# Kernel tuning notes

Measured on AMD Instinct MI355X. Metric: run time of the kernel, lower is better.

The kernel has to match this reference:

```python
import jax, jax.numpy as jnp
import numpy as np

IN_FEATURES = 4096
UNITS = 4096
BATCH = 8192
DENSITY = 0.1
NNZ = int(DENSITY * IN_FEATURES * UNITS)  # 1677721


def _make_indices(rng):
    """Mimic full='output' index construction: each column gets
    NNZ//UNITS distinct random rows; a random 'remain' subset of columns
    gets one extra row. Indices are unique (no duplicates)."""
    k = NNZ // UNITS
    rem = NNZ % UNITS
    # random row permutation per column: argsort of uniform noise
    perm = np.argsort(rng.random((UNITS, IN_FEATURES)), axis=1)
    rows_base = perm[:, :k].reshape(-1)                      # [UNITS*k]
    cols_base = np.repeat(np.arange(UNITS), k)               # [UNITS*k]
    rem_cols = rng.choice(UNITS, rem, replace=False)
    rows_extra = perm[rem_cols, k]
    rows = np.concatenate([rows_base, rows_extra]).astype(np.int32)
    cols = np.concatenate([cols_base, rem_cols]).astype(np.int32)
    return rows, cols


def setup_inputs() -> dict:
    rng = np.random.default_rng(0)
    rows, cols = _make_indices(rng)
    key = jax.random.key(0)
    k1, k2 = jax.random.split(key)
    x = jax.random.normal(k1, (BATCH, IN_FEATURES), dtype=jnp.float32)
    # glorot-uniform-ish scale for the sparse values
    kernel = jax.random.normal(k2, (NNZ,), dtype=jnp.float32) * 0.02
    bias = jnp.zeros((UNITS,), dtype=jnp.float32)
    return {"x": x, "kernel": kernel, "bias": bias,
            "rows": jnp.asarray(rows), "cols": jnp.asarray(cols)}


def reference(x, kernel, bias, rows, cols):
    in_features = x.shape[-1]
    units = bias.shape[0]
    # Scatter sparse COO values into the dense [in, units] weight
    # (indices are unique, so .set is exact), then dense matmul ==
    # tf.sparse.sparse_dense_matmul with the same values/indices.
    W = jnp.zeros((in_features, units), dtype=x.dtype).at[rows, cols].set(kernel)
    out = x @ W + bias
    return jax.nn.relu(out)
```

## Files before the change

kernel.cpp:

```cpp
#include <hip/hip_runtime.h>
#include <hip/hip_bf16.h>

typedef __bf16 bf16;
typedef __attribute__((ext_vector_type(8))) __bf16 bf16x8;
typedef __attribute__((ext_vector_type(4))) __bf16 bf16x4;
typedef __attribute__((ext_vector_type(4))) float f32x4;

#define IN_F 4096
#define UNITS 4096
#define BATCH 8192
#define NNZ_CNT 1677721

#define BM 128
#define BN 128
#define BK 32
#define GK IN_F

#define GLOAD_LDS16(g, l)                                              \
  __builtin_amdgcn_global_load_lds(                                    \
      (const __attribute__((address_space(1))) void*)(g),              \
      (__attribute__((address_space(3))) void*)(l), 16, 0, 0)

__global__ __launch_bounds__(256) void scatter_w_kernel(
    const float* __restrict__ vals, const int* __restrict__ rows,
    const int* __restrict__ cols, bf16* __restrict__ Wt) {
  int i = blockIdx.x * 256 + threadIdx.x;
  if (i < NNZ_CNT) {
    Wt[(size_t)cols[i] * IN_F + rows[i]] = (bf16)vals[i];
  }
}

__global__ __launch_bounds__(256) void cvt_x_kernel(
    const float* __restrict__ x, bf16* __restrict__ xb) {
  size_t i = ((size_t)blockIdx.x * 256 + threadIdx.x) * 4;
  float4 v = *(const float4*)(x + i);
  bf16x4 b;
  b.x = (bf16)v.x;
  b.y = (bf16)v.y;
  b.z = (bf16)v.z;
  b.w = (bf16)v.w;
  *(bf16x4*)(xb + i) = b;
}

__global__ __launch_bounds__(256) void gemm_bias_relu_kernel(
    const bf16* __restrict__ A, const bf16* __restrict__ Bt,
    const float* __restrict__ bias, float* __restrict__ C) {
  __shared__ bf16 As[BM * BK];
  __shared__ bf16 Bs[BN * BK];

  const int tid = threadIdx.x;
  const int lane = tid & 63;
  const int wave = tid >> 6;
  const int wm = wave >> 1;
  const int wn = wave & 1;

  const long m0 = (long)blockIdx.y * BM;
  const long n0 = (long)blockIdx.x * BN;

  const int e0 = tid;
  const int e1 = tid + 256;
  const bf16* gA0 = A + (m0 + (e0 >> 2)) * (long)GK + (e0 & 3) * 8;
  const bf16* gA1 = A + (m0 + (e1 >> 2)) * (long)GK + (e1 & 3) * 8;
  const bf16* gB0 = Bt + (n0 + (e0 >> 2)) * (long)GK + (e0 & 3) * 8;
  const bf16* gB1 = Bt + (n0 + (e1 >> 2)) * (long)GK + (e1 & 3) * 8;

  const int frow = lane & 15;
  const int fk = (lane >> 4) * 8;
  const bf16* lA = As + (wm * 64 + frow) * BK + fk;
  const bf16* lB = Bs + (wn * 64 + frow) * BK + fk;

  f32x4 acc[4][4] = {};

  for (int kt = 0; kt < GK; kt += BK) {
    __syncthreads();
    GLOAD_LDS16(gA0 + kt, As + e0 * 8);
    GLOAD_LDS16(gA1 + kt, As + e1 * 8);
    GLOAD_LDS16(gB0 + kt, Bs + e0 * 8);
    GLOAD_LDS16(gB1 + kt, Bs + e1 * 8);
    __syncthreads();

    bf16x8 af[4], bfr[4];
#pragma unroll
    for (int i = 0; i < 4; ++i) af[i] = *(const bf16x8*)(lA + i * 16 * BK);
#pragma unroll
    for (int i = 0; i < 4; ++i) bfr[i] = *(const bf16x8*)(lB + i * 16 * BK);

#pragma unroll
    for (int im = 0; im < 4; ++im)
#pragma unroll
      for (int in = 0; in < 4; ++in)
        acc[im][in] = __builtin_amdgcn_mfma_f32_16x16x32_bf16(
            af[im], bfr[in], acc[im][in], 0, 0, 0);
  }

  const int crow = (lane >> 4) * 4;
  const int ccol = lane & 15;
#pragma unroll
  for (int in = 0; in < 4; ++in) {
    const long n = n0 + wn * 64 + in * 16 + ccol;
    const float bv = bias[n];
#pragma unroll
    for (int im = 0; im < 4; ++im) {
      const long mbase = m0 + wm * 64 + im * 16 + crow;
#pragma unroll
      for (int i = 0; i < 4; ++i) {
        float v = acc[im][in][i] + bv;
        C[(mbase + i) * UNITS + n] = v > 0.f ? v : 0.f;
      }
    }
  }
}

extern "C" void kernel_launch(void* const* d_in, const int* in_sizes, int n_in,
                              void* d_out, int out_size, void* d_ws,
                              size_t ws_size, hipStream_t stream) {
  const float* x = (const float*)d_in[0];
  const float* kern = (const float*)d_in[1];
  const float* bias = (const float*)d_in[2];
  const int* rows = (const int*)d_in[3];
  const int* cols = (const int*)d_in[4];
  float* out = (float*)d_out;

  bf16* Wt = (bf16*)d_ws;
  bf16* xb = (bf16*)((char*)d_ws + (size_t)UNITS * IN_F * sizeof(bf16));

  hipMemsetAsync(Wt, 0, (size_t)UNITS * IN_F * sizeof(bf16), stream);

  scatter_w_kernel<<<(NNZ_CNT + 255) / 256, 256, 0, stream>>>(kern, rows, cols,
                                                              Wt);

  cvt_x_kernel<<<(size_t)BATCH * IN_F / 4 / 256, 256, 0, stream>>>(x, xb);

  dim3 grid(UNITS / BN, BATCH / BM);
  gemm_bias_relu_kernel<<<grid, 256, 0, stream>>>(xb, Wt, bias, out);
}
```

Before: 575.3 us.

## Replace GEMM with 256x256-tile 8-wave double-buffered pipelined kernel

Swaps the simple 128x128 single-buffered GEMM for a 256x256-tile kernel using 8 waves, XOR-swizzled LDS, and double-buffered global-to-LDS staging. Loads are interleaved with MFMA quads and paced by explicit barriers, vmcnt waits and setprio. Blocks are remapped for L2 locality and the x-conversion kernel now handles 8 elements per thread. It uses 128KB of LDS per block, which limits occupancy, and its correctness depends on the hand-written wait and barrier sequence.

```diff
diff --git a/kernel.cpp b/kernel.cpp
--- a/kernel.cpp
+++ b/kernel.cpp
@@ -3,23 +3,24 @@
 
 typedef __bf16 bf16;
 typedef __attribute__((ext_vector_type(8))) __bf16 bf16x8;
-typedef __attribute__((ext_vector_type(4))) __bf16 bf16x4;
 typedef __attribute__((ext_vector_type(4))) float f32x4;
 
 #define IN_F 4096
 #define UNITS 4096
 #define BATCH 8192
 #define NNZ_CNT 1677721
-
-#define BM 128
-#define BN 128
-#define BK 32
-#define GK IN_F
+#define NT 64
+#define NITER 32
 
 #define GLOAD_LDS16(g, l)                                              \
   __builtin_amdgcn_global_load_lds(                                    \
       (const __attribute__((address_space(1))) void*)(g),              \
       (__attribute__((address_space(3))) void*)(l), 16, 0, 0)
+
+#define S_BARRIER() asm volatile("s_barrier" ::: "memory")
+#define VMCNT4() asm volatile("s_waitcnt vmcnt(4)" ::: "memory")
+#define PRIO1() __builtin_amdgcn_s_setprio(1)
+#define PRIO0() __builtin_amdgcn_s_setprio(0)
 
 __global__ __launch_bounds__(256) void scatter_w_kernel(
     const float* __restrict__ vals, const int* __restrict__ rows,
@@ -30,85 +31,160 @@
   }
 }
 
-__global__ __launch_bounds__(256) void cvt_x_kernel(
-    const float* __restrict__ x, bf16* __restrict__ xb) {
-  size_t i = ((size_t)blockIdx.x * 256 + threadIdx.x) * 4;
-  float4 v = *(const float4*)(x + i);
-  bf16x4 b;
-  b.x = (bf16)v.x;
-  b.y = (bf16)v.y;
-  b.z = (bf16)v.z;
-  b.w = (bf16)v.w;
-  *(bf16x4*)(xb + i) = b;
-}
-
-__global__ __launch_bounds__(256) void gemm_bias_relu_kernel(
+__global__ __launch_bounds__(256) void cvt_x_kernel(const float* __restrict__ x,
+                                                    bf16* __restrict__ xb) {
+  size_t i = ((size_t)blockIdx.x * 256 + threadIdx.x) * 8;
+  float4 v0 = *(const float4*)(x + i);
+  float4 v1 = *(const float4*)(x + i + 4);
+  bf16x8 o;
+  o[0] = (bf16)v0.x; o[1] = (bf16)v0.y; o[2] = (bf16)v0.z; o[3] = (bf16)v0.w;
+  o[4] = (bf16)v1.x; o[5] = (bf16)v1.y; o[6] = (bf16)v1.z; o[7] = (bf16)v1.w;
+  *(bf16x8*)(xb + i) = o;
+}
+
+__device__ __forceinline__ void stage2(const bf16* s0, bf16* l, int tid) {
+  GLOAD_LDS16(s0, l + tid * 8);
+  GLOAD_LDS16(s0 + 128 * (long)IN_F, l + 4096 + tid * 8);
+}
+
+template <int MH, int NH>
+__device__ __forceinline__ void mfma_quad(const bf16x8 (&a)[8],
+                                          const bf16x8 (&b)[2][4],
+                                          f32x4 (&acc)[8][4]) {
+#pragma unroll
+  for (int im = 0; im < 4; ++im)
+#pragma unroll
+    for (int in = 0; in < 2; ++in)
+#pragma unroll
+      for (int ks = 0; ks < 2; ++ks)
+        acc[MH * 4 + im][NH * 2 + in] =
+            __builtin_amdgcn_mfma_f32_16x16x32_bf16(
+                a[im * 2 + ks], b[NH][in * 2 + ks],
+                acc[MH * 4 + im][NH * 2 + in], 0, 0, 0);
+}
+
+__global__ __launch_bounds__(512, 2) void gemm8_kernel(
     const bf16* __restrict__ A, const bf16* __restrict__ Bt,
     const float* __restrict__ bias, float* __restrict__ C) {
-  __shared__ bf16 As[BM * BK];
-  __shared__ bf16 Bs[BN * BK];
+  __shared__ bf16 lds[65536];
 
   const int tid = threadIdx.x;
   const int lane = tid & 63;
   const int wave = tid >> 6;
-  const int wm = wave >> 1;
-  const int wn = wave & 1;
-
-  const long m0 = (long)blockIdx.y * BM;
-  const long n0 = (long)blockIdx.x * BN;
-
-  const int e0 = tid;
-  const int e1 = tid + 256;
-  const bf16* gA0 = A + (m0 + (e0 >> 2)) * (long)GK + (e0 & 3) * 8;
-  const bf16* gA1 = A + (m0 + (e1 >> 2)) * (long)GK + (e1 & 3) * 8;
-  const bf16* gB0 = Bt + (n0 + (e0 >> 2)) * (long)GK + (e0 & 3) * 8;
-  const bf16* gB1 = Bt + (n0 + (e1 >> 2)) * (long)GK + (e1 & 3) * 8;
-
-  const int frow = lane & 15;
-  const int fk = (lane >> 4) * 8;
-  const bf16* lA = As + (wm * 64 + frow) * BK + fk;
-  const bf16* lB = Bs + (wn * 64 + frow) * BK + fk;
-
-  f32x4 acc[4][4] = {};
-
-  for (int kt = 0; kt < GK; kt += BK) {
-    __syncthreads();
-    GLOAD_LDS16(gA0 + kt, As + e0 * 8);
-    GLOAD_LDS16(gA1 + kt, As + e1 * 8);
-    GLOAD_LDS16(gB0 + kt, Bs + e0 * 8);
-    GLOAD_LDS16(gB1 + kt, Bs + e1 * 8);
-    __syncthreads();
-
-    bf16x8 af[4], bfr[4];
-#pragma unroll
-    for (int i = 0; i < 4; ++i) af[i] = *(const bf16x8*)(lA + i * 16 * BK);
-#pragma unroll
-    for (int i = 0; i < 4; ++i) bfr[i] = *(const bf16x8*)(lB + i * 16 * BK);
-
-#pragma unroll
-    for (int im = 0; im < 4; ++im)
-#pragma unroll
-      for (int in = 0; in < 4; ++in)
-        acc[im][in] = __builtin_amdgcn_mfma_f32_16x16x32_bf16(
-            af[im], bfr[in], acc[im][in], 0, 0, 0);
-  }
-
-  const int crow = (lane >> 4) * 4;
-  const int ccol = lane & 15;
-#pragma unroll
-  for (int in = 0; in < 4; ++in) {
-    const long n = n0 + wn * 64 + in * 16 + ccol;
+  const int wm = wave >> 2;
+  const int wn = wave & 3;
+
+  const int sb = (blockIdx.x & 7) * 64 + (blockIdx.x >> 3);
+  const long m0 = (long)(sb & 31) * 256;
+  const long n0 = (long)(sb >> 5) * 256;
+
+  const int q = tid >> 3;
+  const int kx = ((tid & 7) << 3) ^ ((q & 7) << 3);
+  const bf16* gA = A + (m0 + q) * (long)IN_F + kx;
+  const bf16* gB = Bt + (n0 + (q >> 5) * 64 + (q & 31)) * (long)IN_F + kx;
+
+  const int kA0 = (((lane >> 4) << 3) ^ ((lane & 7) << 3));
+  const int baseA = (wm * 64 + (lane & 15)) * 64;
+  const int baseB = (wn * 32 + (lane & 15)) * 64;
+
+  bf16x8 a[8];
+  bf16x8 b[2][4];
+  f32x4 acc[8][4] = {};
+
+#define LDSA(buf, h) (lds + ((buf) * 4 + (h)) * 8192)
+#define LDSB(buf, h) (lds + ((buf) * 4 + 2 + (h)) * 8192)
+#define STAGE_A(buf, h, kt) \
+  stage2(gA + (h) * 64 * (long)IN_F + (kt) * 64, LDSA(buf, h), tid)
+#define STAGE_B(buf, h, kt) \
+  stage2(gB + (h) * 32 * (long)IN_F + (kt) * 64, LDSB(buf, h), tid)
+#define LOAD_A(buf, mh)                                                   \
+  {                                                                       \
+    const bf16* _p = LDSA(buf, mh) + baseA;                               \
+    _Pragma("unroll") for (int im = 0; im < 4; ++im)                      \
+        _Pragma("unroll") for (int ks = 0; ks < 2; ++ks)                  \
+            a[im * 2 + ks] =                                              \
+        *(const bf16x8*)(_p + im * 1024 + (kA0 ^ (ks << 5)));             \
+  }
+#define LOAD_B(buf)                                                       \
+  {                                                                       \
+    _Pragma("unroll") for (int nh = 0; nh < 2; ++nh) {                    \
+      const bf16* _p = LDSB(buf, nh) + baseB;                             \
+      _Pragma("unroll") for (int in = 0; in < 2; ++in)                    \
+          _Pragma("unroll") for (int ks = 0; ks < 2; ++ks)                \
+              b[nh][in * 2 + ks] =                                        \
+          *(const bf16x8*)(_p + in * 1024 + (kA0 ^ (ks << 5)));           \
+    }                                                                     \
+  }
+
+  STAGE_A(0, 0, 0);
+  STAGE_A(0, 1, 0);
+  STAGE_B(0, 0, 0);
+  STAGE_B(0, 1, 0);
+  STAGE_A(1, 0, 1);
+  STAGE_B(1, 0, 1);
+  VMCNT4();
+  S_BARRIER();
+
+  for (int i = 0; i < NITER; ++i) {
+    const int t1 = 2 * i + 1;
+    const int t2 = (2 * i + 2) & (NT - 1);
+    const int t3 = (2 * i + 3) & (NT - 1);
+
+    LOAD_A(0, 0); LOAD_B(0);
+    STAGE_A(1, 1, t1);
+    S_BARRIER(); PRIO1(); mfma_quad<0, 0>(a, b, acc); PRIO0(); S_BARRIER();
+
+    STAGE_B(1, 1, t1);
+    S_BARRIER(); PRIO1(); mfma_quad<0, 1>(a, b, acc); PRIO0(); S_BARRIER();
+
+    LOAD_A(0, 1);
+    STAGE_A(0, 0, t2);
+    S_BARRIER(); PRIO1(); mfma_quad<1, 0>(a, b, acc); PRIO0(); S_BARRIER();
+
+    STAGE_B(0, 0, t2);
+    S_BARRIER(); PRIO1(); mfma_quad<1, 1>(a, b, acc); PRIO0();
+    VMCNT4();
+    S_BARRIER();
+
+    LOAD_A(1, 0); LOAD_B(1);
+    STAGE_A(0, 1, t2);
+    S_BARRIER(); PRIO1(); mfma_quad<0, 0>(a, b, acc); PRIO0(); S_BARRIER();
+
+    STAGE_B(0, 1, t2);
+    S_BARRIER(); PRIO1(); mfma_quad<0, 1>(a, b, acc); PRIO0(); S_BARRIER();
+
+    LOAD_A(1, 1);
+    STAGE_A(1, 0, t3);
+    S_BARRIER(); PRIO1(); mfma_quad<1, 0>(a, b, acc); PRIO0(); S_BARRIER();
+
+    STAGE_B(1, 0, t3);
+    S_BARRIER(); PRIO1(); mfma_quad<1, 1>(a, b, acc); PRIO0();
+    VMCNT4();
+    S_BARRIER();
+  }
+
+#pragma unroll
+  for (int ni = 0; ni < 4; ++ni) {
+    const long n = n0 + wn * 64 + (ni >> 1) * 32 + (ni & 1) * 16 + (lane & 15);
     const float bv = bias[n];
 #pragma unroll
-    for (int im = 0; im < 4; ++im) {
-      const long mbase = m0 + wm * 64 + im * 16 + crow;
-#pragma unroll
-      for (int i = 0; i < 4; ++i) {
-        float v = acc[im][in][i] + bv;
-        C[(mbase + i) * UNITS + n] = v > 0.f ? v : 0.f;
+    for (int mi = 0; mi < 8; ++mi) {
+      const long mrow =
+          m0 + wm * 128 + (mi >> 2) * 64 + (mi & 3) * 16 + ((lane >> 4) << 2);
+      float* cp = C + mrow * UNITS + n;
+#pragma unroll
+      for (int ii = 0; ii < 4; ++ii) {
+        float v = acc[mi][ni][ii] + bv;
+        cp[(long)ii * UNITS] = v > 0.f ? v : 0.f;
       }
     }
   }
+#undef LDSA
+#undef LDSB
+#undef STAGE_A
+#undef STAGE_B
+#undef LOAD_A
+#undef LOAD_B
 }
 
 extern "C" void kernel_launch(void* const* d_in, const int* in_sizes, int n_in,
@@ -125,12 +201,9 @@
   bf16* xb = (bf16*)((char*)d_ws + (size_t)UNITS * IN_F * sizeof(bf16));
 
   hipMemsetAsync(Wt, 0, (size_t)UNITS * IN_F * sizeof(bf16), stream);
-
   scatter_w_kernel<<<(NNZ_CNT + 255) / 256, 256, 0, stream>>>(kern, rows, cols,
                                                               Wt);
-
-  cvt_x_kernel<<<(size_t)BATCH * IN_F / 4 / 256, 256, 0, stream>>>(x, xb);
-
-  dim3 grid(UNITS / BN, BATCH / BM);
-  gemm_bias_relu_kernel<<<grid, 256, 0, stream>>>(xb, Wt, bias, out);
-}
+  cvt_x_kernel<<<(size_t)BATCH * IN_F / 8 / 256, 256, 0, stream>>>(x, xb);
+
+  gemm8_kernel<<<512, 512, 0, stream>>>(xb, Wt, bias, out);
+}
```

New measurement: 467.6 us. -18.7%, faster.
